# Kernel tuning notes

Measured on AMD Instinct MI355X. Metric: run time of the kernel, lower is better.

The kernel has to match this reference:

```python
import jax, jax.numpy as jnp
import numpy as np

HIDDEN = 4096
N_EXPERTS = 128
TOP_K = 8
N_GROUP = 1
TOPK_GROUP = 1
ROUTED_SCALING = 1.0
NORM_TOPK_PROB = True


def setup_inputs() -> dict:
    key = jax.random.key(0)
    k1, k2 = jax.random.split(key)
    tokens = 16384  # batch 4 * seq 4096
    hidden_states = jax.random.normal(k1, (tokens, HIDDEN), dtype=jnp.float32)
    # router gate weight (n_routed_experts, hidden_size)
    weight = jax.random.normal(k2, (N_EXPERTS, HIDDEN), dtype=jnp.float32) * 0.02
    # e_score_correction_bias buffer, initialized to zeros in the module
    e_score_correction_bias = jnp.zeros((N_EXPERTS,), dtype=jnp.float32)
    return {"hidden_states": hidden_states, "weight": weight,
            "e_score_correction_bias": e_score_correction_bias}


def _get_topk_indices(scores, bias):
    # scores: [T, E] sigmoid gate scores; bias: [E]
    T = scores.shape[0]
    experts_per_group = N_EXPERTS // N_GROUP
    s = scores + bias[None, :]  # scores_for_choice
    # group score: sum of top-2 corrected scores within each group
    grp = s.reshape(T, N_GROUP, experts_per_group)
    group_scores = jnp.sum(jax.lax.top_k(grp, 2)[0], axis=-1)  # [T, G]
    group_idx = jax.lax.top_k(group_scores, TOPK_GROUP)[1]      # [T, topk_group]
    group_mask = jnp.zeros((T, N_GROUP), dtype=bool).at[
        jnp.arange(T)[:, None], group_idx].set(True)
    score_mask = jnp.repeat(group_mask, experts_per_group, axis=-1)  # [T, E]
    s_masked = jnp.where(score_mask, s, 0.0)
    topk_indices = jax.lax.top_k(s_masked, TOP_K)[1]  # [T, top_k]
    return topk_indices


def reference(hidden_states, weight, e_score_correction_bias):
    x = hidden_states.reshape(-1, HIDDEN).astype(jnp.float32)
    router_logits = x @ weight.astype(jnp.float32).T          # [T, E]
    scores = jax.nn.sigmoid(router_logits)
    topk_indices = _get_topk_indices(scores, e_score_correction_bias)
    topk_weights = jnp.take_along_axis(scores, topk_indices, axis=1)  # [T, top_k]
    if NORM_TOPK_PROB:
        denom = jnp.sum(topk_weights, axis=-1, keepdims=True) + 1e-20
        topk_weights = topk_weights / denom
    topk_weights = topk_weights * ROUTED_SCALING
    return topk_indices, topk_weights
```

## Files before the change

kernel.cpp:

```cpp
#include <hip/hip_runtime.h>
#include <math.h>

#define HIDDEN 4096
#define NEXP   128
#define TOPK   8
#define BT     32
#define CHUNK  64
#define NCHUNK (HIDDEN / CHUNK)
#define SSTR   132
#define PLANE  (NEXP * CHUNK)

typedef int v4i __attribute__((ext_vector_type(4)));

static __device__ __forceinline__ unsigned pack4(int a, int b, int c, int d) {
    return (unsigned)(a & 255) | ((unsigned)(b & 255) << 8) |
           ((unsigned)(c & 255) << 16) | ((unsigned)(d & 255) << 24);
}

static __device__ __forceinline__ void slice5(float val, float scale1,
        int& d0, int& d1, int& d2, int& d3, int& d4) {
    float v = val * scale1;
    float f = __builtin_rintf(v);
    float r = v - f;
    int nh = (int)f;
    int nl = (int)__builtin_rintf(r * 2097152.0f);
    d0 = (nh + 64) >> 7;  d1 = nh - (d0 << 7);
    d2 = (nl + 8192) >> 14;
    int r2 = nl - (d2 << 14);
    d3 = (r2 + 64) >> 7;  d4 = r2 - (d3 << 7);
}

static __device__ __forceinline__ void slice4(float val, float scale1,
        int& d0, int& d1, int& d2, int& d3) {
    float v = val * scale1;
    float f = __builtin_rintf(v);
    float r = v - f;
    int nh = (int)f;
    int nl = (int)__builtin_rintf(r * 16384.0f);
    d0 = (nh + 64) >> 7;  d1 = nh - (d0 << 7);
    d2 = (nl + 64) >> 7;  d3 = nl - (d2 << 7);
}

__global__ __launch_bounds__(256)
void slice_w_kernel(const float* __restrict__ W, signed char* __restrict__ P)
{
    const int t  = blockIdx.x * 256 + threadIdx.x;
    const int e  = t >> 9;
    const int k0 = (t & 511) * 8;
    const float* src = W + (size_t)e * HIDDEN + k0;
    const float4 a = ((const float4*)src)[0];
    const float4 b = ((const float4*)src)[1];

    int p00,p01,p02,p03,p04; slice5(a.x, 32768.0f, p00,p01,p02,p03,p04);
    int p10,p11,p12,p13,p14; slice5(a.y, 32768.0f, p10,p11,p12,p13,p14);
    int p20,p21,p22,p23,p24; slice5(a.z, 32768.0f, p20,p21,p22,p23,p24);
    int p30,p31,p32,p33,p34; slice5(a.w, 32768.0f, p30,p31,p32,p33,p34);
    int p40,p41,p42,p43,p44; slice5(b.x, 32768.0f, p40,p41,p42,p43,p44);
    int p50,p51,p52,p53,p54; slice5(b.y, 32768.0f, p50,p51,p52,p53,p54);
    int p60,p61,p62,p63,p64; slice5(b.z, 32768.0f, p60,p61,p62,p63,p64);
    int p70,p71,p72,p73,p74; slice5(b.w, 32768.0f, p70,p71,p72,p73,p74);

    const int c = k0 >> 6, kin = k0 & 63;
    signed char* base = P + ((size_t)(c * 5) * NEXP + e) * CHUNK + kin;
    uint2 v;
    v.x = pack4(p00,p10,p20,p30); v.y = pack4(p40,p50,p60,p70);
    *(uint2*)(base + 0 * PLANE) = v;
    v.x = pack4(p01,p11,p21,p31); v.y = pack4(p41,p51,p61,p71);
    *(uint2*)(base + 1 * PLANE) = v;
    v.x = pack4(p02,p12,p22,p32); v.y = pack4(p42,p52,p62,p72);
    *(uint2*)(base + 2 * PLANE) = v;
    v.x = pack4(p03,p13,p23,p33); v.y = pack4(p43,p53,p63,p73);
    *(uint2*)(base + 3 * PLANE) = v;
    v.x = pack4(p04,p14,p24,p34); v.y = pack4(p44,p54,p64,p74);
    *(uint2*)(base + 4 * PLANE) = v;
}

static __device__ __forceinline__ void slice_store_x(char* dst, float4 xa, float4 xb)
{
    int a00,a01,a02,a03; slice4(xa.x, 1024.0f, a00,a01,a02,a03);
    int a10,a11,a12,a13; slice4(xa.y, 1024.0f, a10,a11,a12,a13);
    int a20,a21,a22,a23; slice4(xa.z, 1024.0f, a20,a21,a22,a23);
    int a30,a31,a32,a33; slice4(xa.w, 1024.0f, a30,a31,a32,a33);
    int a40,a41,a42,a43; slice4(xb.x, 1024.0f, a40,a41,a42,a43);
    int a50,a51,a52,a53; slice4(xb.y, 1024.0f, a50,a51,a52,a53);
    int a60,a61,a62,a63; slice4(xb.z, 1024.0f, a60,a61,a62,a63);
    int a70,a71,a72,a73; slice4(xb.w, 1024.0f, a70,a71,a72,a73);
    uint2 v;
    v.x = pack4(a00,a10,a20,a30); v.y = pack4(a40,a50,a60,a70);
    *(uint2*)(dst + 0 * 2048) = v;
    v.x = pack4(a01,a11,a21,a31); v.y = pack4(a41,a51,a61,a71);
    *(uint2*)(dst + 1 * 2048) = v;
    v.x = pack4(a02,a12,a22,a32); v.y = pack4(a42,a52,a62,a72);
    *(uint2*)(dst + 2 * 2048) = v;
    v.x = pack4(a03,a13,a23,a33); v.y = pack4(a43,a53,a63,a73);
    *(uint2*)(dst + 3 * 2048) = v;
}

__global__ __launch_bounds__(256, 2)
void router_kernel(const float* __restrict__ X,
                   const signed char* __restrict__ P,
                   const float* __restrict__ Bias,
                   float* __restrict__ Out, int T)
{
    __shared__ double S[BT * SSTR];
    char* Ast = (char*)S;

    const int tid  = threadIdx.x;
    const int lane = tid & 63;
    const int wave = tid >> 6;
    const int tokBase = blockIdx.x * BT;

    const int sm  = tid & 31;
    const int sk8 = tid >> 5;
    int srow = tokBase + sm; if (srow >= T) srow = T - 1;
    const float* xptr = X + (size_t)srow * HIDDEN + sk8 * 8;
    const int su    = sm * 4 + (sk8 >> 1);
    const int swoff = ((su ^ ((su >> 3) & 7)) << 4) + (sk8 & 1) * 8;

    const int ru0  = ((lane & 15)     ) * 4 + (lane >> 4);
    const int ru1  = ((lane & 15) + 16) * 4 + (lane >> 4);
    const int rph0 = (ru0 ^ ((ru0 >> 3) & 7)) << 4;
    const int rph1 = (ru1 ^ ((ru1 >> 3) & 7)) << 4;

    const int eb0 = wave * 32 + (lane & 15);
    const int koff = (lane >> 4) * 16;
    const size_t boff0 = (size_t)eb0 * CHUNK + koff;
    const size_t boff1 = boff0 + (size_t)16 * CHUNK;

    v4i acc[2][2][5];
    #pragma unroll
    for (int tt = 0; tt < 2; tt++)
        #pragma unroll
        for (int et = 0; et < 2; et++)
            #pragma unroll
            for (int s = 0; s < 5; s++)
                acc[tt][et][s] = (v4i){0,0,0,0};

    float4 xa = ((const float4*)xptr)[0];
    float4 xb = ((const float4*)xptr)[1];
    slice_store_x(Ast + swoff, xa, xb);
    __syncthreads();

    for (int c = 0; c < NCHUNK; c++) {
        const int buf = (c & 1) * 8192;
        if (c + 1 < NCHUNK) {
            const float* nx = xptr + (c + 1) * CHUNK;
            xa = ((const float4*)nx)[0];
            xb = ((const float4*)nx)[1];
        }
        const signed char* pc = P + (size_t)(c * 5) * PLANE;
        v4i bf[2][5];
        #pragma unroll
        for (int s = 0; s < 5; s++) {
            bf[0][s] = *(const v4i*)(pc + (size_t)s * PLANE + boff0);
            bf[1][s] = *(const v4i*)(pc + (size_t)s * PLANE + boff1);
        }
        #pragma unroll
        for (int tt = 0; tt < 2; tt++) {
            const char* ap = Ast + buf + (tt ? rph1 : rph0);
            const v4i a0 = *(const v4i*)(ap + 0 * 2048);
            const v4i a1 = *(const v4i*)(ap + 1 * 2048);
            const v4i a2 = *(const v4i*)(ap + 2 * 2048);
            const v4i a3 = *(const v4i*)(ap + 3 * 2048);
            #pragma unroll
            for (int et = 0; et < 2; et++) {
                acc[tt][et][0] = __builtin_amdgcn_mfma_i32_16x16x64_i8(a0, bf[et][0], acc[tt][et][0], 0, 0, 0);
                acc[tt][et][1] = __builtin_amdgcn_mfma_i32_16x16x64_i8(a0, bf[et][1], acc[tt][et][1], 0, 0, 0);
                acc[tt][et][1] = __builtin_amdgcn_mfma_i32_16x16x64_i8(a1, bf[et][0], acc[tt][et][1], 0, 0, 0);
                acc[tt][et][2] = __builtin_amdgcn_mfma_i32_16x16x64_i8(a0, bf[et][2], acc[tt][et][2], 0, 0, 0);
                acc[tt][et][2] = __builtin_amdgcn_mfma_i32_16x16x64_i8(a1, bf[et][1], acc[tt][et][2], 0, 0, 0);
                acc[tt][et][2] = __builtin_amdgcn_mfma_i32_16x16x64_i8(a2, bf[et][0], acc[tt][et][2], 0, 0, 0);
                acc[tt][et][3] = __builtin_amdgcn_mfma_i32_16x16x64_i8(a0, bf[et][3], acc[tt][et][3], 0, 0, 0);
                acc[tt][et][3] = __builtin_amdgcn_mfma_i32_16x16x64_i8(a1, bf[et][2], acc[tt][et][3], 0, 0, 0);
                acc[tt][et][3] = __builtin_amdgcn_mfma_i32_16x16x64_i8(a2, bf[et][1], acc[tt][et][3], 0, 0, 0);
                acc[tt][et][3] = __builtin_amdgcn_mfma_i32_16x16x64_i8(a3, bf[et][0], acc[tt][et][3], 0, 0, 0);
                acc[tt][et][4] = __builtin_amdgcn_mfma_i32_16x16x64_i8(a0, bf[et][4], acc[tt][et][4], 0, 0, 0);
                acc[tt][et][4] = __builtin_amdgcn_mfma_i32_16x16x64_i8(a1, bf[et][3], acc[tt][et][4], 0, 0, 0);
                acc[tt][et][4] = __builtin_amdgcn_mfma_i32_16x16x64_i8(a2, bf[et][2], acc[tt][et][4], 0, 0, 0);
                acc[tt][et][4] = __builtin_amdgcn_mfma_i32_16x16x64_i8(a3, bf[et][1], acc[tt][et][4], 0, 0, 0);
            }
        }
        if (c + 1 < NCHUNK)
            slice_store_x(Ast + (buf ^ 8192) + swoff, xa, xb);
        __syncthreads();
    }

    {
        const double w0 = 0x1p-11, w1 = 0x1p-18, w2 = 0x1p-25, w3 = 0x1p-32, w4 = 0x1p-39;
        #pragma unroll
        for (int tt = 0; tt < 2; tt++)
            #pragma unroll
            for (int et = 0; et < 2; et++) {
                const int ecol = wave * 32 + et * 16 + (lane & 15);
                const double bias = (double)Bias[ecol];
                #pragma unroll
                for (int r = 0; r < 4; r++) {
                    const int trow = tt * 16 + (lane >> 4) * 4 + r;
                    const double logit = (double)acc[tt][et][0][r] * w0
                                       + (double)acc[tt][et][1][r] * w1
                                       + (double)acc[tt][et][2][r] * w2
                                       + (double)acc[tt][et][3][r] * w3
                                       + (double)acc[tt][et][4][r] * w4;
                    S[trow * SSTR + ecol] = 1.0 / (1.0 + exp(-logit)) + bias;
                }
            }
    }
    __syncthreads();

    if (tid < BT) {
        const int tok = tokBase + tid;
        if (tok < T) {
            double* row = S + tid * SSTR;
            int    cidx[TOPK];
            double csc[TOPK];
            #pragma unroll
            for (int p = 0; p < TOPK; p++) {
                double best = -1e300; int bi = 0;
                for (int e = 0; e < NEXP; e++) {
                    const double v = row[e];
                    if (v > best) { best = v; bi = e; }
                }
                cidx[p] = bi; csc[p] = best; row[bi] = -1e300;
            }
            double sum = 0.0, wts[TOPK];
            #pragma unroll
            for (int p = 0; p < TOPK; p++) {
                const double sg = csc[p] - (double)Bias[cidx[p]];
                wts[p] = sg; sum += sg;
            }
            const double inv = 1.0 / (sum + 1e-20);
            float* oi = Out + (size_t)tok * TOPK;
            float* ow = Out + (size_t)T * TOPK + (size_t)tok * TOPK;
            #pragma unroll
            for (int p = 0; p < TOPK; p++) {
                oi[p] = (float)cidx[p];
                ow[p] = (float)(wts[p] * inv);
            }
        }
    }
}

extern "C" void kernel_launch(void* const* d_in, const int* in_sizes, int n_in,
                              void* d_out, int out_size, void* d_ws, size_t ws_size,
                              hipStream_t stream) {
    const float* X    = (const float*)d_in[0];
    const float* W    = (const float*)d_in[1];
    const float* Bias = (const float*)d_in[2];
    float* Out = (float*)d_out;
    const int T = in_sizes[0] / HIDDEN;
    signed char* P = (signed char*)d_ws;

    hipLaunchKernelGGL(slice_w_kernel, dim3(NEXP * 512 / 256), dim3(256), 0, stream, W, P);
    hipLaunchKernelGGL(router_kernel, dim3((T + BT - 1) / BT), dim3(256), 0, stream,
                       X, P, Bias, Out, T);
}
```

Baseline: 453.1 us.

## Prefetch weight planes a chunk ahead and parallelize top-k across eight lanes

The K loop is unrolled by two with ping-pong register buffers, so each chunk's weight-plane fragments are loaded from global memory one chunk before the MFMAs that use them. This hides load latency behind matrix work, but doubles the B-fragment register footprint under a 2-blocks-per-SM launch bound. The top-k epilogue, which ran serially on 32 threads scanning 128 experts, now uses all 256 threads: each holds 16 experts and an 8-lane xor-shuffle reduction picks each winner, breaking ties toward the lower index.

```diff
diff --git a/kernel.cpp b/kernel.cpp
--- a/kernel.cpp
+++ b/kernel.cpp
@@ -96,6 +96,35 @@
     *(uint2*)(dst + 3 * 2048) = v;
 }
 
+#define MFMA_BLOCK(BF, BUF)                                                    \
+    {                                                                          \
+        _Pragma("unroll")                                                      \
+        for (int tt = 0; tt < 2; tt++) {                                       \
+            const char* ap = Ast + (BUF) + (tt ? rph1 : rph0);                 \
+            const v4i a0 = *(const v4i*)(ap + 0 * 2048);                       \
+            const v4i a1 = *(const v4i*)(ap + 1 * 2048);                       \
+            const v4i a2 = *(const v4i*)(ap + 2 * 2048);                       \
+            const v4i a3 = *(const v4i*)(ap + 3 * 2048);                       \
+            _Pragma("unroll")                                                  \
+            for (int et = 0; et < 2; et++) {                                   \
+                acc[tt][et][0] = __builtin_amdgcn_mfma_i32_16x16x64_i8(a0, BF[et][0], acc[tt][et][0], 0, 0, 0); \
+                acc[tt][et][1] = __builtin_amdgcn_mfma_i32_16x16x64_i8(a0, BF[et][1], acc[tt][et][1], 0, 0, 0); \
+                acc[tt][et][1] = __builtin_amdgcn_mfma_i32_16x16x64_i8(a1, BF[et][0], acc[tt][et][1], 0, 0, 0); \
+                acc[tt][et][2] = __builtin_amdgcn_mfma_i32_16x16x64_i8(a0, BF[et][2], acc[tt][et][2], 0, 0, 0); \
+                acc[tt][et][2] = __builtin_amdgcn_mfma_i32_16x16x64_i8(a1, BF[et][1], acc[tt][et][2], 0, 0, 0); \
+                acc[tt][et][2] = __builtin_amdgcn_mfma_i32_16x16x64_i8(a2, BF[et][0], acc[tt][et][2], 0, 0, 0); \
+                acc[tt][et][3] = __builtin_amdgcn_mfma_i32_16x16x64_i8(a0, BF[et][3], acc[tt][et][3], 0, 0, 0); \
+                acc[tt][et][3] = __builtin_amdgcn_mfma_i32_16x16x64_i8(a1, BF[et][2], acc[tt][et][3], 0, 0, 0); \
+                acc[tt][et][3] = __builtin_amdgcn_mfma_i32_16x16x64_i8(a2, BF[et][1], acc[tt][et][3], 0, 0, 0); \
+                acc[tt][et][3] = __builtin_amdgcn_mfma_i32_16x16x64_i8(a3, BF[et][0], acc[tt][et][3], 0, 0, 0); \
+                acc[tt][et][4] = __builtin_amdgcn_mfma_i32_16x16x64_i8(a0, BF[et][4], acc[tt][et][4], 0, 0, 0); \
+                acc[tt][et][4] = __builtin_amdgcn_mfma_i32_16x16x64_i8(a1, BF[et][3], acc[tt][et][4], 0, 0, 0); \
+                acc[tt][et][4] = __builtin_amdgcn_mfma_i32_16x16x64_i8(a2, BF[et][2], acc[tt][et][4], 0, 0, 0); \
+                acc[tt][et][4] = __builtin_amdgcn_mfma_i32_16x16x64_i8(a3, BF[et][1], acc[tt][et][4], 0, 0, 0); \
+            }                                                                  \
+        }                                                                      \
+    }
+
 __global__ __launch_bounds__(256, 2)
 void router_kernel(const float* __restrict__ X,
                    const signed char* __restrict__ P,
@@ -139,50 +168,53 @@
     float4 xa = ((const float4*)xptr)[0];
     float4 xb = ((const float4*)xptr)[1];
     slice_store_x(Ast + swoff, xa, xb);
+
+    v4i bfA[2][5], bfB[2][5];
+    #pragma unroll
+    for (int s = 0; s < 5; s++) {
+        bfA[0][s] = *(const v4i*)(P + (size_t)s * PLANE + boff0);
+        bfA[1][s] = *(const v4i*)(P + (size_t)s * PLANE + boff1);
+    }
     __syncthreads();
 
-    for (int c = 0; c < NCHUNK; c++) {
-        const int buf = (c & 1) * 8192;
-        if (c + 1 < NCHUNK) {
+    #pragma unroll 1
+    for (int c = 0; c < NCHUNK; c += 2) {
+        {
+            const signed char* pn = P + (size_t)((c + 1) * 5) * PLANE;
+            #pragma unroll
+            for (int s = 0; s < 5; s++) {
+                bfB[0][s] = *(const v4i*)(pn + (size_t)s * PLANE + boff0);
+                bfB[1][s] = *(const v4i*)(pn + (size_t)s * PLANE + boff1);
+            }
             const float* nx = xptr + (c + 1) * CHUNK;
             xa = ((const float4*)nx)[0];
             xb = ((const float4*)nx)[1];
+
+            MFMA_BLOCK(bfA, 0)
+
+            slice_store_x(Ast + 8192 + swoff, xa, xb);
+            __syncthreads();
         }
-        const signed char* pc = P + (size_t)(c * 5) * PLANE;
-        v4i bf[2][5];
-        #pragma unroll
-        for (int s = 0; s < 5; s++) {
-            bf[0][s] = *(const v4i*)(pc + (size_t)s * PLANE + boff0);
-            bf[1][s] = *(const v4i*)(pc + (size_t)s * PLANE + boff1);
+        {
+            if (c + 2 < NCHUNK) {
+                const signed char* pn = P + (size_t)((c + 2) * 5) * PLANE;
+                #pragma unroll
+                for (int s = 0; s < 5; s++) {
+                    bfA[0][s] = *(const v4i*)(pn + (size_t)s * PLANE + boff0);
+                    bfA[1][s] = *(const v4i*)(pn + (size_t)s * PLANE + boff1);
+                }
+                const float* nx = xptr + (c + 2) * CHUNK;
+                xa = ((const float4*)nx)[0];
+                xb = ((const float4*)nx)[1];
+            }
+
+            MFMA_BLOCK(bfB, 8192)
+
+            if (c + 2 < NCHUNK) {
+                slice_store_x(Ast + swoff, xa, xb);
+            }
+            __syncthreads();
         }
-        #pragma unroll
-        for (int tt = 0; tt < 2; tt++) {
-            const char* ap = Ast + buf + (tt ? rph1 : rph0);
-            const v4i a0 = *(const v4i*)(ap + 0 * 2048);
-            const v4i a1 = *(const v4i*)(ap + 1 * 2048);
-            const v4i a2 = *(const v4i*)(ap + 2 * 2048);
-            const v4i a3 = *(const v4i*)(ap + 3 * 2048);
-            #pragma unroll
-            for (int et = 0; et < 2; et++) {
-                acc[tt][et][0] = __builtin_amdgcn_mfma_i32_16x16x64_i8(a0, bf[et][0], acc[tt][et][0], 0, 0, 0);
-                acc[tt][et][1] = __builtin_amdgcn_mfma_i32_16x16x64_i8(a0, bf[et][1], acc[tt][et][1], 0, 0, 0);
-                acc[tt][et][1] = __builtin_amdgcn_mfma_i32_16x16x64_i8(a1, bf[et][0], acc[tt][et][1], 0, 0, 0);
-                acc[tt][et][2] = __builtin_amdgcn_mfma_i32_16x16x64_i8(a0, bf[et][2], acc[tt][et][2], 0, 0, 0);
-                acc[tt][et][2] = __builtin_amdgcn_mfma_i32_16x16x64_i8(a1, bf[et][1], acc[tt][et][2], 0, 0, 0);
-                acc[tt][et][2] = __builtin_amdgcn_mfma_i32_16x16x64_i8(a2, bf[et][0], acc[tt][et][2], 0, 0, 0);
-                acc[tt][et][3] = __builtin_amdgcn_mfma_i32_16x16x64_i8(a0, bf[et][3], acc[tt][et][3], 0, 0, 0);
-                acc[tt][et][3] = __builtin_amdgcn_mfma_i32_16x16x64_i8(a1, bf[et][2], acc[tt][et][3], 0, 0, 0);
-                acc[tt][et][3] = __builtin_amdgcn_mfma_i32_16x16x64_i8(a2, bf[et][1], acc[tt][et][3], 0, 0, 0);
-                acc[tt][et][3] = __builtin_amdgcn_mfma_i32_16x16x64_i8(a3, bf[et][0], acc[tt][et][3], 0, 0, 0);
-                acc[tt][et][4] = __builtin_amdgcn_mfma_i32_16x16x64_i8(a0, bf[et][4], acc[tt][et][4], 0, 0, 0);
-                acc[tt][et][4] = __builtin_amdgcn_mfma_i32_16x16x64_i8(a1, bf[et][3], acc[tt][et][4], 0, 0, 0);
-                acc[tt][et][4] = __builtin_amdgcn_mfma_i32_16x16x64_i8(a2, bf[et][2], acc[tt][et][4], 0, 0, 0);
-                acc[tt][et][4] = __builtin_amdgcn_mfma_i32_16x16x64_i8(a3, bf[et][1], acc[tt][et][4], 0, 0, 0);
-            }
-        }
-        if (c + 1 < NCHUNK)
-            slice_store_x(Ast + (buf ^ 8192) + swoff, xa, xb);
-        __syncthreads();
     }
 
     {
@@ -207,33 +239,47 @@
     }
     __syncthreads();
 
-    if (tid < BT) {
-        const int tok = tokBase + tid;
-        if (tok < T) {
-            double* row = S + tid * SSTR;
-            int    cidx[TOPK];
-            double csc[TOPK];
-            #pragma unroll
-            for (int p = 0; p < TOPK; p++) {
-                double best = -1e300; int bi = 0;
-                for (int e = 0; e < NEXP; e++) {
-                    const double v = row[e];
-                    if (v > best) { best = v; bi = e; }
-                }
-                cidx[p] = bi; csc[p] = best; row[bi] = -1e300;
-            }
-            double sum = 0.0, wts[TOPK];
-            #pragma unroll
-            for (int p = 0; p < TOPK; p++) {
-                const double sg = csc[p] - (double)Bias[cidx[p]];
-                wts[p] = sg; sum += sg;
-            }
-            const double inv = 1.0 / (sum + 1e-20);
+    {
+        const int tk  = tid >> 3;
+        const int j   = tid & 7;
+        const int tok = tokBase + tk;
+        const double* row = S + tk * SSTR + j * 16;
+        double v[16];
+        #pragma unroll
+        for (int k = 0; k < 16; k++) v[k] = row[k];
+
+        double wts[TOPK]; float idxf[TOPK];
+        double wsum = 0.0;
+        #pragma unroll
+        for (int p = 0; p < TOPK; p++) {
+            double best = v[0]; int bi = 0;
+            #pragma unroll
+            for (int k = 1; k < 16; k++)
+                if (v[k] > best) { best = v[k]; bi = k; }
+            int be = j * 16 + bi;
+            #pragma unroll
+            for (int off = 1; off < 8; off <<= 1) {
+                double ob = __shfl_xor(best, off, 8);
+                int    oe = __shfl_xor(be,   off, 8);
+                if (ob > best || (ob == best && oe < be)) { best = ob; be = oe; }
+            }
+            const bool own = (be >> 4) == j;
+            const int  bl  = be & 15;
+            #pragma unroll
+            for (int k = 0; k < 16; k++)
+                if (own && k == bl) v[k] = -1.0e300;
+            const double sg = best - (double)Bias[be];
+            wts[p]  = sg;
+            wsum   += sg;
+            idxf[p] = (float)be;
+        }
+        if (j == 0 && tok < T) {
+            const double inv = 1.0 / (wsum + 1e-20);
             float* oi = Out + (size_t)tok * TOPK;
             float* ow = Out + (size_t)T * TOPK + (size_t)tok * TOPK;
             #pragma unroll
             for (int p = 0; p < TOPK; p++) {
-                oi[p] = (float)cidx[p];
+                oi[p] = idxf[p];
                 ow[p] = (float)(wts[p] * inv);
             }
         }
```

Result: no change. 449.2 us (-0.9%).
